# Performance work log

Measured on AMD Instinct MI355X. Metric: run time of the kernel, lower is better.

The kernel has to match this reference:

```python
import jax, jax.numpy as jnp
import numpy as np
import math

N = 100000      # num_of_nodes
E = 1600000     # edges (~avg degree 16)
F = 128         # node_feature
D = 128         # node_hidden (also topK pool size)
NR = 90000      # remaining nodes
L = 2           # num_conv_layer
LAMDA = 0.5
ALPHA = 0.1


def setup_inputs() -> dict:
    key = jax.random.key(0)
    ks = jax.random.split(key, 12)
    g = lambda k, s: jax.random.normal(k, s, jnp.float32) * 0.05
    perm = np.random.RandomState(0).permutation(N)  # disjoint remain/added split
    return {
        "x": jax.random.normal(ks[0], (N, F), jnp.float32),
        "node_scores": jax.random.normal(ks[1], (N,), jnp.float32),
        "W_hid": g(ks[2], (F, D)), "b_hid": jnp.zeros((D,), jnp.float32),
        "Wl": g(ks[3], (D, D)), "bl": jnp.zeros((D,), jnp.float32),
        "Wr": g(ks[4], (D, D)), "br": jnp.zeros((D,), jnp.float32),
        "a": g(ks[5], (1, D)),
        "h0_w": g(ks[6], (D, D)),              # initial_weight (GRU hidden init / GCN weight)
        "W_ih": g(ks[7], (3 * D, D)), "W_hh": g(ks[8], (3 * D, D)),
        "b_ih": jnp.zeros((3 * D,), jnp.float32), "b_hh": jnp.zeros((3 * D,), jnp.float32),
        "edge_index": jax.random.randint(ks[9], (2, E), 0, N),
        "remain_nodes_index": jnp.asarray(perm[:NR], jnp.int32),
        "added_nodes_index": jnp.asarray(perm[NR:], jnp.int32),
        "node_id": jnp.arange(N, dtype=jnp.int32),
    }


def _gru_step(x_in, h, W_ih, W_hh, b_ih, b_hh):
    # torch nn.GRU single step, gate order (r, z, n)
    gx = x_in @ W_ih.T + b_ih
    gh = h @ W_hh.T + b_hh
    xr, xz, xn = jnp.split(gx, 3, axis=-1)
    hr, hz, hn = jnp.split(gh, 3, axis=-1)
    r = jax.nn.sigmoid(xr + hr)
    z = jax.nn.sigmoid(xz + hz)
    n = jnp.tanh(xn + r * hn)
    return (1.0 - z) * n + z * h


def _edge_softmax_weights(edge_index, a, h_l, h_r):
    # _dynamic_self_attention_v2: per-edge scores normalized over src rows
    src, dst = edge_index[0], edge_index[1]
    al = (jax.nn.leaky_relu(h_l, 0.2) * a).sum(-1)   # [N]
    ar = (jax.nn.leaky_relu(h_r, 0.2) * a).sum(-1)   # [N]
    e = al[src] + ar[dst]                            # [E]
    e = jnp.exp(e - e.max())
    rowsum = jax.ops.segment_sum(e, src, num_segments=h_l.shape[0])
    return e / (rowsum[src] + 1e-16)


def _spmm_adj_t(edge_index, w, feats):
    # (A_trans @ feats)[i] = sum over edges with dst==i of w_e * feats[src]
    src, dst = edge_index[0], edge_index[1]
    return jax.ops.segment_sum(w[:, None] * feats[src], dst, num_segments=feats.shape[0])


def reference(x, node_scores, W_hid, b_hid, Wl, bl, Wr, br, a, h0_w, W_ih, W_hh, b_ih, b_hh, edge_index, remain_nodes_index, added_nodes_index, node_id):
    h = jax.nn.relu(x @ W_hid + b_hid)                 # [N, D]
    remain_nodes = node_id[remain_nodes_index]
    remain_x = h[remain_nodes_index]
    added_nodes = node_id[added_nodes_index]
    added_x = h[added_nodes_index]
    scores = node_scores[remain_nodes_index]
    X_res = jnp.zeros((N, D), h.dtype)
    X_res = X_res.at[remain_nodes].set(remain_x).at[added_nodes].set(added_x)
    # topK pooling branch (N > D and NR > D statically)
    _, topk = jax.lax.top_k(scores, D)
    X_pool = remain_x[topk]                            # [D, D]: GRU batch=D, feat=D
    pooling_node = remain_nodes[topk]
    h_new = _gru_step(X_pool, h0_w, W_ih, W_hh, b_ih, b_hh)  # [D, D]
    # torch: X_GCN = X_residual (alias) then in-place scatter -> both updated
    X_res = X_res.at[pooling_node].set(h_new)
    X_gcn = X_res
    Wl_X = jax.nn.relu(X_gcn @ Wl + bl)
    Wr_X = jax.nn.relu(X_gcn @ Wr + br)
    w_edge = _edge_softmax_weights(edge_index, a, Wl_X, Wr_X)
    out = X_gcn
    for l in range(1, L + 1):
        theta = math.log(LAMDA / l + 1.0)
        hi = _spmm_adj_t(edge_index, w_edge, out)
        support = (1.0 - ALPHA) * hi + ALPHA * X_res
        out = jax.nn.relu(theta * (support @ h_new) + (1.0 - theta) * support)
    return out
```

## Files before the change

kernel.cpp:

```cpp
#include <hip/hip_runtime.h>

typedef unsigned int u32;
typedef unsigned short u16;
typedef unsigned long long u64;

#define DD 128
#define ELLW 64
#define NB 196
#define BSH 9
#define BCAP 12288

typedef __attribute__((ext_vector_type(8))) short short8;
typedef __attribute__((ext_vector_type(4))) float f32x4;
union fragu { uint4 q; short8 s; };

__device__ __forceinline__ u32 mono32(float f) {
    u32 u = __float_as_uint(f);
    return (u & 0x80000000u) ? ~u : (u | 0x80000000u);
}
__device__ __forceinline__ u16 f2bf(float f) {
    u32 u = __float_as_uint(f);
    u32 r = (u + 0x7FFFu + ((u >> 16) & 1u)) >> 16;
    return (u16)r;
}
__device__ __forceinline__ float bflo(u32 p) { return __uint_as_float(p << 16); }
__device__ __forceinline__ float bfhi(u32 p) { return __uint_as_float(p & 0xFFFF0000u); }
__device__ __forceinline__ u32 packbf(float a, float b) {
    return (u32)f2bf(a) | ((u32)f2bf(b) << 16);
}

__device__ u32 block_incl_scan(u32 v, u32* wsum ) {
    int t = threadIdx.x, lane = t & 63, wid = t >> 6;
    u32 sc = v;
#pragma unroll
    for (int off = 1; off < 64; off <<= 1) {
        u32 n1 = __shfl_up(sc, off);
        if (lane >= off) sc += n1;
    }
    if (lane == 63) wsum[wid] = sc;
    __syncthreads();
    if (t < 16) {
        u32 wv = wsum[t];
#pragma unroll
        for (int off = 1; off < 16; off <<= 1) {
            u32 n1 = __shfl_up(wv, off, 16);
            if ((t & 15) >= off) wv += n1;
        }
        wsum[t] = wv;
    }
    __syncthreads();
    u32 r = sc + (wid ? wsum[wid - 1] : 0u);
    __syncthreads();
    return r;
}

template <int MODE, int ABF, int EAR>
__global__ __launch_bounds__(256) void k_mfma(
    const void* __restrict__ Ain, const u32* __restrict__ resid,
    const float* __restrict__ B, const float* __restrict__ bias,
    const float* __restrict__ av, const float* __restrict__ scaleS,
    u16* __restrict__ outBF, float* __restrict__ outF, float* __restrict__ outS,
    float theta, int N) {
    __shared__ alignas(16) unsigned char As[64 * 256];
    __shared__ float spart[64];
    int t = threadIdx.x, lane = t & 63, wave = t >> 6;
    int R0 = blockIdx.x * 64;
    int brow = (lane >> 4) * 8;
    int bcol0 = wave * 32 + (lane & 15);
    fragu bfr[2][4];
#pragma unroll
    for (int ntl = 0; ntl < 2; ++ntl)
#pragma unroll
        for (int ks = 0; ks < 4; ++ks) {
            u16 h[8];
#pragma unroll
            for (int i = 0; i < 8; ++i)
                h[i] = f2bf(B[(size_t)(ks * 32 + brow + i) * 128 + bcol0 + ntl * 16]);
            bfr[ntl][ks].q = make_uint4((u32)h[0] | ((u32)h[1] << 16), (u32)h[2] | ((u32)h[3] << 16),
                                        (u32)h[4] | ((u32)h[5] << 16), (u32)h[6] | ((u32)h[7] << 16));
        }
    float bc[2] = {0.f, 0.f}, ac[2] = {0.f, 0.f};
    if (MODE == 0) {
#pragma unroll
        for (int ntl = 0; ntl < 2; ++ntl) {
            bc[ntl] = bias[bcol0 + ntl * 16];
            if (EAR) ac[ntl] = av[bcol0 + ntl * 16];
        }
    }
    if (EAR && t < 64) spart[t] = 0.f;
#pragma unroll
    for (int q2 = 0; q2 < 4; ++q2) {
        int c = t + q2 * 256;
        int row = c >> 4, c16 = c & 15;
        uint4 v = make_uint4(0u, 0u, 0u, 0u);
        if (R0 + row < N) {
            if (ABF == 1) {
                v = ((const uint4*)Ain)[(size_t)(R0 + row) * 16 + c16];
            } else if (ABF == 2) {
                uint4 pv = ((const uint4*)Ain)[(size_t)(R0 + row) * 16 + c16];
                uint4 xv = ((const uint4*)resid)[(size_t)(R0 + row) * 16 + c16];
                v.x = packbf(bflo(pv.x) + 0.1f * bflo(xv.x), bfhi(pv.x) + 0.1f * bfhi(xv.x));
                v.y = packbf(bflo(pv.y) + 0.1f * bflo(xv.y), bfhi(pv.y) + 0.1f * bfhi(xv.y));
                v.z = packbf(bflo(pv.z) + 0.1f * bflo(xv.z), bfhi(pv.z) + 0.1f * bfhi(xv.z));
                v.w = packbf(bflo(pv.w) + 0.1f * bflo(xv.w), bfhi(pv.w) + 0.1f * bfhi(xv.w));
            } else {
                float4 f0 = ((const float4*)Ain)[(size_t)(R0 + row) * 32 + c16 * 2];
                float4 f1 = ((const float4*)Ain)[(size_t)(R0 + row) * 32 + c16 * 2 + 1];
                v.x = packbf(f0.x, f0.y);
                v.y = packbf(f0.z, f0.w);
                v.z = packbf(f1.x, f1.y);
                v.w = packbf(f1.z, f1.w);
            }
        }
        *(uint4*)(As + row * 256 + ((c16 * 16) ^ ((row & 7) << 4))) = v;
    }
    __syncthreads();
    int arow = lane & 15, agrp = lane >> 4;
    float om = 1.f - theta;
#pragma unroll
    for (int rs = 0; rs < 4; ++rs) {
        int rl = rs * 16 + arow;
        fragu afr[4];
#pragma unroll
        for (int ks = 0; ks < 4; ++ks)
            afr[ks].q = *(const uint4*)(As + rl * 256 + ((ks * 64 + agrp * 16) ^ ((rl & 7) << 4)));
        float part[4] = {0.f, 0.f, 0.f, 0.f};
#pragma unroll
        for (int ntl = 0; ntl < 2; ++ntl) {
            f32x4 acc = {0.f, 0.f, 0.f, 0.f};
#pragma unroll
            for (int ks = 0; ks < 4; ++ks)
                acc = __builtin_amdgcn_mfma_f32_16x16x32_bf16(afr[ks].s, bfr[ntl][ks].s, acc, 0, 0, 0);
            int colg = wave * 32 + ntl * 16 + (lane & 15);
#pragma unroll
            for (int r = 0; r < 4; ++r) {
                int rowg = R0 + rs * 16 + agrp * 4 + r;
                if (MODE == 0) {
                    float v = fmaxf(acc[r] + bc[ntl], 0.f);
                    if (rowg < N) outBF[(size_t)rowg * 128 + colg] = f2bf(v);
                    if (EAR) part[r] += v * ac[ntl];
                } else {
                    int rl2 = rs * 16 + agrp * 4 + r;
                    u16 rh = *(const u16*)(As + rl2 * 256 + ((colg * 2) ^ ((rl2 & 7) << 4)));
                    float resv = __uint_as_float((u32)rh << 16);
                    float v = fmaxf(theta * acc[r] + om * resv, 0.f);
                    if (rowg < N) {
                        if (MODE == 2) {
                            float rsc = 1.f / (scaleS[rowg] + 1e-30f);
                            outBF[(size_t)rowg * 128 + colg] = f2bf(v * rsc);
                        } else {
                            outF[(size_t)rowg * 128 + colg] = v;
                        }
                    }
                }
            }
        }
        if (EAR) {
#pragma unroll
            for (int r = 0; r < 4; ++r) {
                float s = part[r];
                s += __shfl_xor(s, 1); s += __shfl_xor(s, 2);
                s += __shfl_xor(s, 4); s += __shfl_xor(s, 8);
                if ((lane & 15) == 0) atomicAdd(&spart[rs * 16 + agrp * 4 + r], s);
            }
        }
    }
    if (EAR) {
        __syncthreads();
        if (t < 64 && R0 + t < N) outS[R0 + t] = expf(spart[t]);
    }
}

__global__ __launch_bounds__(256) void k_spmm(
    const u32* __restrict__ feat, const float* __restrict__ ear,
    const u32* __restrict__ cnt, const int* __restrict__ ell,
    u32* __restrict__ P, int N) {
    int w = (int)((blockIdx.x * (u32)blockDim.x + threadIdx.x) >> 6);
    int lane = threadIdx.x & 63;
    if (w >= N) return;
    int m = (int)min(cnt[w], (u32)ELLW);
    int sv = (lane < m) ? ell[((size_t)w << 6) + lane] : 0;
    float a0 = 0.f, a1 = 0.f;
    int j = 0;
    for (; j + 16 <= m; j += 16) {
        u32 pv[16];
#pragma unroll
        for (int q = 0; q < 16; ++q) {
            int s = __shfl(sv, j + q);
            pv[q] = feat[(size_t)s * 64 + lane];
        }
#pragma unroll
        for (int q = 0; q < 16; ++q) { a0 += bflo(pv[q]); a1 += bfhi(pv[q]); }
    }
    for (; j + 8 <= m; j += 8) {
        u32 pv[8];
#pragma unroll
        for (int q = 0; q < 8; ++q) {
            int s = __shfl(sv, j + q);
            pv[q] = feat[(size_t)s * 64 + lane];
        }
#pragma unroll
        for (int q = 0; q < 8; ++q) { a0 += bflo(pv[q]); a1 += bfhi(pv[q]); }
    }
    for (; j + 2 <= m; j += 2) {
        int s0 = __shfl(sv, j + 0), s1 = __shfl(sv, j + 1);
        u32 p0 = feat[(size_t)s0 * 64 + lane];
        u32 p1 = feat[(size_t)s1 * 64 + lane];
        a0 += bflo(p0) + bflo(p1);
        a1 += bfhi(p0) + bfhi(p1);
    }
    if (j < m) {
        int s0 = __shfl(sv, j);
        u32 p0 = feat[(size_t)s0 * 64 + lane];
        a0 += bflo(p0);
        a1 += bfhi(p0);
    }
    float sc = 0.9f * ear[w];
    P[(size_t)w * 64 + lane] = packbf(sc * a0, sc * a1);
}

__global__ __launch_bounds__(256) void k_bucket(
    const int* __restrict__ ei, u32* __restrict__ bD, u32* __restrict__ bS,
    u32* __restrict__ curD, u32* __restrict__ curS, int E, int nblocks) {
    __shared__ u32 cnt0[NB], cnt1[NB], pos0[NB], pos1[NB], base0[NB], base1[NB];
    int t = threadIdx.x;
    int chunk = (E + nblocks - 1) / nblocks;
    int e0 = blockIdx.x * chunk, e1 = min(E, e0 + chunk);
    for (int i = t; i < NB; i += 256) { cnt0[i] = 0; cnt1[i] = 0; pos0[i] = 0; pos1[i] = 0; }
    __syncthreads();
    for (int e = e0 + t; e < e1; e += 256) {
        int s = ei[e], d = ei[E + e];
        atomicAdd(&cnt0[d >> BSH], 1u);
        atomicAdd(&cnt1[s >> BSH], 1u);
    }
    __syncthreads();
    for (int i = t; i < NB; i += 256) {
        base0[i] = atomicAdd(&curD[i], cnt0[i]);
        base1[i] = atomicAdd(&curS[i], cnt1[i]);
    }
    __syncthreads();
    for (int e = e0 + t; e < e1; e += 256) {
        int s = ei[e], d = ei[E + e];
        int bd = d >> BSH, bs = s >> BSH;
        u32 pD = base0[bd] + atomicAdd(&pos0[bd], 1u);
        u32 pS = base1[bs] + atomicAdd(&pos1[bs], 1u);
        if (pD < (u32)BCAP) bD[(size_t)bd * BCAP + pD] = ((u32)(d & 511) << 17) | (u32)s;
        if (pS < (u32)BCAP) bS[(size_t)bs * BCAP + pS] = ((u32)(s & 511) << 17) | (u32)d;
    }
}

__global__ __launch_bounds__(256) void k_ellSsc(
    const u32* __restrict__ bD, const u32* __restrict__ bS,
    const u32* __restrict__ curD, const u32* __restrict__ curS,
    const float* __restrict__ ear, const u32* __restrict__ Xrbf,
    int* __restrict__ ell, u32* __restrict__ cnt,
    float* __restrict__ S, u32* __restrict__ Xsc, int N) {
    __shared__ u32 lcnt[512];
    __shared__ float ls[512];
    int t = threadIdx.x;
    if (blockIdx.x < NB) {
        int b = blockIdx.x;
        for (int i = t; i < 512; i += 256) lcnt[i] = 0;
        __syncthreads();
        u32 beg = (u32)b * BCAP, end = beg + min(curD[b], (u32)BCAP);
        for (u32 e = beg + t; e < end; e += 256) {
            u32 p = bD[e];
            int dloc = (int)(p >> 17), s = (int)(p & 0x1FFFFu);
            u32 q = atomicAdd(&lcnt[dloc], 1u);
            if (q < (u32)ELLW) ell[(((size_t)(b << BSH) + dloc) << 6) + q] = s;
        }
        __syncthreads();
        int r0 = b << BSH;
        for (int i = t; i < 512; i += 256) {
            int row = r0 + i;
            if (row < N) cnt[row] = min(lcnt[i], (u32)ELLW);
        }
    } else {
        int b = blockIdx.x - NB;
        for (int i = t; i < 512; i += 256) ls[i] = 0.f;
        __syncthreads();
        u32 beg = (u32)b * BCAP, end = beg + min(curS[b], (u32)BCAP);
        for (u32 e = beg + t; e < end; e += 256) {
            u32 p = bS[e];
            int sloc = (int)(p >> 17), d = (int)(p & 0x1FFFFu);
            atomicAdd(&ls[sloc], ear[d]);
        }
        __syncthreads();
        int r0 = b << BSH;
        for (int i = t; i < 512; i += 256) {
            int row = r0 + i;
            if (row < N) S[row] = ls[i];
        }
        int rows = min(512, N - r0);
        if (rows <= 0) return;
        for (int idx = t; idx < rows * 64; idx += 256) {
            int rl = idx >> 6, c = idx & 63;
            int row = r0 + rl;
            float rs = 1.f / (ls[rl] + 1e-30f);
            u32 p = Xrbf[(size_t)row * 64 + c];
            Xsc[(size_t)row * 64 + c] = packbf(bflo(p) * rs, bfhi(p) * rs);
        }
    }
}

__global__ void k_hist(const float* __restrict__ scores, const int* __restrict__ remain,
                       u32* __restrict__ hist, int NR) {
    int i = blockIdx.x * blockDim.x + threadIdx.x;
    if (i < NR) atomicAdd(&hist[mono32(scores[remain[i]]) >> 16], 1u);
}

__global__ void k_cutoff(const u32* __restrict__ hist, u32* __restrict__ misc, int K) {
    __shared__ u32 wsum[16];
    __shared__ u32 carry_s, found_s;
    int t = threadIdx.x;
    if (t == 0) { carry_s = 0; found_s = 0; }
    __syncthreads();
    for (int c = 0; c < 64; ++c) {
        int key = 65535 - ((c << 10) + t);
        u32 v = hist[key];
        u32 carry = carry_s;
        __syncthreads();
        u32 incl = block_incl_scan(v, wsum);
        u32 mycum = carry + incl;
        u32 myprev = mycum - v;
        if (mycum >= (u32)K && myprev < (u32)K) {
            misc[2] = (u32)key;
            misc[3] = myprev;
            found_s = 1;
        }
        if (t == 1023) carry_s = mycum;
        __syncthreads();
        if (found_s) return;
    }
}

__global__ void k_collect(const float* __restrict__ scores, const int* __restrict__ remain,
                          const u32* __restrict__ misc, int* __restrict__ cand,
                          u32* __restrict__ cand_cnt, int NR, int CMAX) {
    u32 B = misc[2];
    int i = blockIdx.x * blockDim.x + threadIdx.x;
    if (i < NR) {
        u32 b = mono32(scores[remain[i]]) >> 16;
        if (b >= B) {
            u32 p = atomicAdd(cand_cnt, 1u);
            if (p < (u32)CMAX) cand[p] = i;
        }
    }
}

__global__ void k_select(const float* __restrict__ scores, const int* __restrict__ remain,
                         const u32* __restrict__ misc, const int* __restrict__ cand,
                         int* __restrict__ pooling, int K, int CMAX) {
    __shared__ u64 keys[4096];
    int n = (int)min(misc[0], (u32)CMAX);
    int t = threadIdx.x;
    for (int c = t; c < n; c += 1024) {
        int i = cand[c];
        u32 m = mono32(scores[remain[i]]);
        keys[c] = ((u64)m << 32) | (u64)(0xFFFFFFFFu - (u32)i);
    }
    __syncthreads();
    for (int c = t; c < n; c += 1024) {
        u64 myk = keys[c];
        int rank = 0;
        for (int j = 0; j < n; ++j) rank += (keys[j] > myk) ? 1 : 0;
        if (rank < K) pooling[rank] = remain[cand[c]];
    }
}

__global__ void k_gru(u32* __restrict__ Xr_bf, const int* __restrict__ pooling,
                      const float* __restrict__ h0w, const float* __restrict__ Wih,
                      const float* __restrict__ Whh, const float* __restrict__ bih,
                      const float* __restrict__ bhh, const float* __restrict__ Wr,
                      const float* __restrict__ br, const float* __restrict__ av,
                      float* __restrict__ hnew, float* __restrict__ ear) {
    __shared__ float xrow[DD], hrow[DD], hn[DD];
    __shared__ float red[2];
    int j = blockIdx.x, t = threadIdx.x;
    int node = pooling[j];
    xrow[t] = __uint_as_float((u32)((const u16*)Xr_bf)[(size_t)node * DD + t] << 16);
    hrow[t] = h0w[j * DD + t];
    __syncthreads();
    float gx[3], gh[3];
#pragma unroll
    for (int g = 0; g < 3; ++g) {
        const float* wi = Wih + (g * DD + t) * DD;
        const float* wh = Whh + (g * DD + t) * DD;
        float ax = bih[g * DD + t];
        float ah = bhh[g * DD + t];
        for (int d = 0; d < DD; ++d) {
            ax += xrow[d] * wi[d];
            ah += hrow[d] * wh[d];
        }
        gx[g] = ax; gh[g] = ah;
    }
    float r = 1.f / (1.f + expf(-(gx[0] + gh[0])));
    float z = 1.f / (1.f + expf(-(gx[1] + gh[1])));
    float nn = tanhf(gx[2] + r * gh[2]);
    float hv = (1.f - z) * nn + z * hrow[t];
    hnew[j * DD + t] = hv;
    hn[t] = hv;
    __syncthreads();
    if (t < 64) Xr_bf[(size_t)node * 64 + t] = packbf(hn[2 * t], hn[2 * t + 1]);
    float acc = br[t];
    for (int k = 0; k < DD; ++k) acc += hn[k] * Wr[k * DD + t];
    float val = fmaxf(acc, 0.f) * av[t];
#pragma unroll
    for (int off = 32; off > 0; off >>= 1) val += __shfl_xor(val, off);
    if ((t & 63) == 0) red[t >> 6] = val;
    __syncthreads();
    if (t == 0) ear[node] = expf(red[0] + red[1]);
}

extern "C" void kernel_launch(void* const* d_in, const int* in_sizes, int n_in,
                              void* d_out, int out_size, void* d_ws, size_t ws_size,
                              hipStream_t stream) {
    const float* x    = (const float*)d_in[0];
    const float* nsc  = (const float*)d_in[1];
    const float* Wh   = (const float*)d_in[2];
    const float* bh   = (const float*)d_in[3];
    const float* Wr   = (const float*)d_in[6];
    const float* br   = (const float*)d_in[7];
    const float* av   = (const float*)d_in[8];
    const float* h0w  = (const float*)d_in[9];
    const float* Wih  = (const float*)d_in[10];
    const float* Whh  = (const float*)d_in[11];
    const float* bih  = (const float*)d_in[12];
    const float* bhh  = (const float*)d_in[13];
    const int* ei     = (const int*)d_in[14];
    const int* remain = (const int*)d_in[15];

    int N = in_sizes[1];
    int E = in_sizes[14] / 2;
    int NR = in_sizes[15];
    const int K = DD;
    const int CMAX = 4096;
    int mblocks = (N + 63) / 64;
    const int NBLK = 512;

    char* ws = (char*)d_ws;
    size_t off = 0;
    auto alloc = [&](size_t bytes) -> size_t {
        off = (off + 255) & ~(size_t)255;
        size_t o = off;
        off += bytes;
        return o;
    };
    size_t bucket_bytes = (size_t)2 * NB * BCAP * 4;
    size_t sup_bytes = (size_t)N * 64 * 4;
    size_t o_Xrbf = alloc((size_t)N * 64 * 4);
    size_t o_Xsc  = alloc((size_t)N * 64 * 4);
    size_t o_Abf  = alloc((size_t)N * 64 * 4);
    size_t o_sup  = alloc(bucket_bytes > sup_bytes ? bucket_bytes : sup_bytes);
    size_t o_ear  = alloc((size_t)N * 4);
    size_t o_ell  = alloc((size_t)N * ELLW * 4);
    size_t o_cand = alloc((size_t)CMAX * 4);
    size_t o_pool = alloc((size_t)K * 4);
    size_t o_hnew = alloc((size_t)DD * DD * 4);
    size_t o_S    = alloc((size_t)N * 4);
    size_t o_cnt  = alloc((size_t)N * 4);
    size_t o_cur  = alloc((size_t)2 * 256 * 4);
    size_t o_hist = alloc((size_t)65536 * 4);
    size_t o_misc = alloc((size_t)64 * 4);
    size_t zero_len = (o_misc + 64 * 4) - o_cur;
    (void)ws_size; (void)n_in; (void)out_size;

    u32*   Xrbf = (u32*)(ws + o_Xrbf);
    u32*   Xsc  = (u32*)(ws + o_Xsc);
    u32*   Abf  = (u32*)(ws + o_Abf);
    u32*   P    = (u32*)(ws + o_sup);
    u32*   bD   = (u32*)(ws + o_sup);
    u32*   bS   = (u32*)(ws + o_sup + (size_t)NB * BCAP * 4);
    float* ear  = (float*)(ws + o_ear);
    int*   ell  = (int*)(ws + o_ell);
    int*   cand = (int*)(ws + o_cand);
    int*   pool = (int*)(ws + o_pool);
    float* hnew = (float*)(ws + o_hnew);
    float* S    = (float*)(ws + o_S);
    u32*   cnt  = (u32*)(ws + o_cnt);
    u32*   curD = (u32*)(ws + o_cur);
    u32*   curS = (u32*)(ws + o_cur + 256 * 4);
    u32*   hist = (u32*)(ws + o_hist);
    u32*   misc = (u32*)(ws + o_misc);

    const float theta1 = 0.40546510810816438f;
    const float theta2 = 0.22314355131420976f;

    hipMemsetAsync(ws + o_cur, 0, zero_len, stream);

    k_mfma<0, 0, 1><<<mblocks, 256, 0, stream>>>(x, nullptr, Wh, bh, av, nullptr,
                                                 (u16*)Xrbf, nullptr, ear, 0.f, N);
    k_hist<<<(NR + 255) / 256, 256, 0, stream>>>(nsc, remain, hist, NR);
    k_cutoff<<<1, 1024, 0, stream>>>(hist, misc, K);
    k_collect<<<(NR + 255) / 256, 256, 0, stream>>>(nsc, remain, misc, cand, misc, NR, CMAX);
    k_select<<<1, 1024, 0, stream>>>(nsc, remain, misc, cand, pool, K, CMAX);
    k_mfma<0, 1, 1><<<mblocks, 256, 0, stream>>>(Xrbf, nullptr, Wr, br, av, nullptr,
                                                 (u16*)Xsc ,
                                                 nullptr, ear, 0.f, N);
    k_gru<<<K, DD, 0, stream>>>(Xrbf, pool, h0w, Wih, Whh, bih, bhh, Wr, br, av, hnew, ear);
    k_bucket<<<NBLK, 256, 0, stream>>>(ei, bD, bS, curD, curS, E, NBLK);
    k_ellSsc<<<2 * NB, 256, 0, stream>>>(bD, bS, curD, curS, ear, Xrbf, ell, cnt, S, Xsc, N);
    k_spmm<<<(N + 3) / 4, 256, 0, stream>>>(Xsc, ear, cnt, ell, P, N);
    k_mfma<2, 2, 0><<<mblocks, 256, 0, stream>>>(P, Xrbf, hnew, nullptr, nullptr, S,
                                                 (u16*)Abf, nullptr, nullptr, theta1, N);
    k_spmm<<<(N + 3) / 4, 256, 0, stream>>>(Abf, ear, cnt, ell, P, N);
    k_mfma<3, 2, 0><<<mblocks, 256, 0, stream>>>(P, Xrbf, hnew, nullptr, nullptr, nullptr,
                                                 nullptr, (float*)d_out, nullptr, theta2, N);
}
```

Before: 384.2 us.

## Fuse hidden and Wr projections; apply inverse row-sum inside SpMM gather

Merges the hidden-layer GEMM and the Wr attention-score GEMM into one kernel that keeps the bf16 hidden tile in shared memory, so the second pass no longer re-reads Xrbf or writes an unused Xsc output. The per-source 1/rowsum scaling is no longer applied by pre-scaling feature copies (the Xsc pass in k_ellSsc and the rescale in the MODE 2 epilogue). Instead each SpMM lane loads invS for its neighbour and the gather uses FMA with a shuffled weight. The 16-wide unrolled gather loop is dropped. This cuts a kernel launch and a full N×128 read/write pass, at the cost of extra invS gathers, shuffles, and some loss of memory-level parallelism in the SpMM.

Measured after the change: 328.4 us (median of 2 runs). 14.5% less time.

```diff
diff --git a/kernel.cpp b/kernel.cpp
--- a/kernel.cpp
+++ b/kernel.cpp
@@ -54,19 +54,18 @@
     return r;
 }
 
-template <int MODE, int ABF, int EAR>
-__global__ __launch_bounds__(256) void k_mfma(
-    const void* __restrict__ Ain, const u32* __restrict__ resid,
-    const float* __restrict__ B, const float* __restrict__ bias,
-    const float* __restrict__ av, const float* __restrict__ scaleS,
-    u16* __restrict__ outBF, float* __restrict__ outF, float* __restrict__ outS,
-    float theta, int N) {
+__global__ __launch_bounds__(256) void k_hid(
+    const float* __restrict__ x, const float* __restrict__ Wh, const float* __restrict__ bh,
+    const float* __restrict__ Wr, const float* __restrict__ br, const float* __restrict__ av,
+    u16* __restrict__ outBF, float* __restrict__ ear, int N) {
     __shared__ alignas(16) unsigned char As[64 * 256];
+    __shared__ alignas(16) unsigned char Xs[64 * 256];
     __shared__ float spart[64];
     int t = threadIdx.x, lane = t & 63, wave = t >> 6;
     int R0 = blockIdx.x * 64;
     int brow = (lane >> 4) * 8;
     int bcol0 = wave * 32 + (lane & 15);
+    if (t < 64) spart[t] = 0.f;
     fragu bfr[2][4];
 #pragma unroll
     for (int ntl = 0; ntl < 2; ++ntl)
@@ -75,48 +74,34 @@
             u16 h[8];
 #pragma unroll
             for (int i = 0; i < 8; ++i)
-                h[i] = f2bf(B[(size_t)(ks * 32 + brow + i) * 128 + bcol0 + ntl * 16]);
+                h[i] = f2bf(Wh[(size_t)(ks * 32 + brow + i) * 128 + bcol0 + ntl * 16]);
             bfr[ntl][ks].q = make_uint4((u32)h[0] | ((u32)h[1] << 16), (u32)h[2] | ((u32)h[3] << 16),
                                         (u32)h[4] | ((u32)h[5] << 16), (u32)h[6] | ((u32)h[7] << 16));
         }
-    float bc[2] = {0.f, 0.f}, ac[2] = {0.f, 0.f};
-    if (MODE == 0) {
-#pragma unroll
-        for (int ntl = 0; ntl < 2; ++ntl) {
-            bc[ntl] = bias[bcol0 + ntl * 16];
-            if (EAR) ac[ntl] = av[bcol0 + ntl * 16];
-        }
-    }
-    if (EAR && t < 64) spart[t] = 0.f;
+    float bc[2], brc[2], avc[2];
+#pragma unroll
+    for (int ntl = 0; ntl < 2; ++ntl) {
+        bc[ntl] = bh[bcol0 + ntl * 16];
+        brc[ntl] = br[bcol0 + ntl * 16];
+        avc[ntl] = av[bcol0 + ntl * 16];
+    }
 #pragma unroll
     for (int q2 = 0; q2 < 4; ++q2) {
         int c = t + q2 * 256;
         int row = c >> 4, c16 = c & 15;
         uint4 v = make_uint4(0u, 0u, 0u, 0u);
         if (R0 + row < N) {
-            if (ABF == 1) {
-                v = ((const uint4*)Ain)[(size_t)(R0 + row) * 16 + c16];
-            } else if (ABF == 2) {
-                uint4 pv = ((const uint4*)Ain)[(size_t)(R0 + row) * 16 + c16];
-                uint4 xv = ((const uint4*)resid)[(size_t)(R0 + row) * 16 + c16];
-                v.x = packbf(bflo(pv.x) + 0.1f * bflo(xv.x), bfhi(pv.x) + 0.1f * bfhi(xv.x));
-                v.y = packbf(bflo(pv.y) + 0.1f * bflo(xv.y), bfhi(pv.y) + 0.1f * bfhi(xv.y));
-                v.z = packbf(bflo(pv.z) + 0.1f * bflo(xv.z), bfhi(pv.z) + 0.1f * bfhi(xv.z));
-                v.w = packbf(bflo(pv.w) + 0.1f * bflo(xv.w), bfhi(pv.w) + 0.1f * bfhi(xv.w));
-            } else {
-                float4 f0 = ((const float4*)Ain)[(size_t)(R0 + row) * 32 + c16 * 2];
-                float4 f1 = ((const float4*)Ain)[(size_t)(R0 + row) * 32 + c16 * 2 + 1];
-                v.x = packbf(f0.x, f0.y);
-                v.y = packbf(f0.z, f0.w);
-                v.z = packbf(f1.x, f1.y);
-                v.w = packbf(f1.z, f1.w);
-            }
+            float4 f0 = ((const float4*)x)[(size_t)(R0 + row) * 32 + c16 * 2];
+            float4 f1 = ((const float4*)x)[(size_t)(R0 + row) * 32 + c16 * 2 + 1];
+            v.x = packbf(f0.x, f0.y);
+            v.y = packbf(f0.z, f0.w);
+            v.z = packbf(f1.x, f1.y);
+            v.w = packbf(f1.z, f1.w);
         }
         *(uint4*)(As + row * 256 + ((c16 * 16) ^ ((row & 7) << 4))) = v;
     }
     __syncthreads();
     int arow = lane & 15, agrp = lane >> 4;
-    float om = 1.f - theta;
 #pragma unroll
     for (int rs = 0; rs < 4; ++rs) {
         int rl = rs * 16 + arow;
@@ -124,7 +109,6 @@
 #pragma unroll
         for (int ks = 0; ks < 4; ++ks)
             afr[ks].q = *(const uint4*)(As + rl * 256 + ((ks * 64 + agrp * 16) ^ ((rl & 7) << 4)));
-        float part[4] = {0.f, 0.f, 0.f, 0.f};
 #pragma unroll
         for (int ntl = 0; ntl < 2; ++ntl) {
             f32x4 acc = {0.f, 0.f, 0.f, 0.f};
@@ -134,86 +118,167 @@
             int colg = wave * 32 + ntl * 16 + (lane & 15);
 #pragma unroll
             for (int r = 0; r < 4; ++r) {
+                int rl2 = rs * 16 + agrp * 4 + r;
+                int rowg = R0 + rl2;
+                float v = fmaxf(acc[r] + bc[ntl], 0.f);
+                u16 hb = f2bf(v);
+                if (rowg < N) outBF[(size_t)rowg * 128 + colg] = hb;
+                *(u16*)(Xs + rl2 * 256 + ((colg * 2) ^ ((rl2 & 7) << 4))) = hb;
+            }
+        }
+    }
+    fragu wfr[2][4];
+#pragma unroll
+    for (int ntl = 0; ntl < 2; ++ntl)
+#pragma unroll
+        for (int ks = 0; ks < 4; ++ks) {
+            u16 h[8];
+#pragma unroll
+            for (int i = 0; i < 8; ++i)
+                h[i] = f2bf(Wr[(size_t)(ks * 32 + brow + i) * 128 + bcol0 + ntl * 16]);
+            wfr[ntl][ks].q = make_uint4((u32)h[0] | ((u32)h[1] << 16), (u32)h[2] | ((u32)h[3] << 16),
+                                        (u32)h[4] | ((u32)h[5] << 16), (u32)h[6] | ((u32)h[7] << 16));
+        }
+    __syncthreads();
+#pragma unroll
+    for (int rs = 0; rs < 4; ++rs) {
+        int rl = rs * 16 + arow;
+        fragu afr[4];
+#pragma unroll
+        for (int ks = 0; ks < 4; ++ks)
+            afr[ks].q = *(const uint4*)(Xs + rl * 256 + ((ks * 64 + agrp * 16) ^ ((rl & 7) << 4)));
+        float part[4] = {0.f, 0.f, 0.f, 0.f};
+#pragma unroll
+        for (int ntl = 0; ntl < 2; ++ntl) {
+            f32x4 acc = {0.f, 0.f, 0.f, 0.f};
+#pragma unroll
+            for (int ks = 0; ks < 4; ++ks)
+                acc = __builtin_amdgcn_mfma_f32_16x16x32_bf16(afr[ks].s, wfr[ntl][ks].s, acc, 0, 0, 0);
+#pragma unroll
+            for (int r = 0; r < 4; ++r)
+                part[r] += fmaxf(acc[r] + brc[ntl], 0.f) * avc[ntl];
+        }
+#pragma unroll
+        for (int r = 0; r < 4; ++r) {
+            float s = part[r];
+            s += __shfl_xor(s, 1); s += __shfl_xor(s, 2);
+            s += __shfl_xor(s, 4); s += __shfl_xor(s, 8);
+            if ((lane & 15) == 0) atomicAdd(&spart[rs * 16 + agrp * 4 + r], s);
+        }
+    }
+    __syncthreads();
+    if (t < 64 && R0 + t < N) ear[R0 + t] = expf(spart[t]);
+}
+
+template <int MODE>
+__global__ __launch_bounds__(256) void k_mfma(
+    const u32* __restrict__ P, const u32* __restrict__ resid,
+    const float* __restrict__ B, u16* __restrict__ outBF, float* __restrict__ outF,
+    float theta, int N) {
+    __shared__ alignas(16) unsigned char As[64 * 256];
+    int t = threadIdx.x, lane = t & 63, wave = t >> 6;
+    int R0 = blockIdx.x * 64;
+    int brow = (lane >> 4) * 8;
+    int bcol0 = wave * 32 + (lane & 15);
+    fragu bfr[2][4];
+#pragma unroll
+    for (int ntl = 0; ntl < 2; ++ntl)
+#pragma unroll
+        for (int ks = 0; ks < 4; ++ks) {
+            u16 h[8];
+#pragma unroll
+            for (int i = 0; i < 8; ++i)
+                h[i] = f2bf(B[(size_t)(ks * 32 + brow + i) * 128 + bcol0 + ntl * 16]);
+            bfr[ntl][ks].q = make_uint4((u32)h[0] | ((u32)h[1] << 16), (u32)h[2] | ((u32)h[3] << 16),
+                                        (u32)h[4] | ((u32)h[5] << 16), (u32)h[6] | ((u32)h[7] << 16));
+        }
+#pragma unroll
+    for (int q2 = 0; q2 < 4; ++q2) {
+        int c = t + q2 * 256;
+        int row = c >> 4, c16 = c & 15;
+        uint4 v = make_uint4(0u, 0u, 0u, 0u);
+        if (R0 + row < N) {
+            uint4 pv = ((const uint4*)P)[(size_t)(R0 + row) * 16 + c16];
+            uint4 xv = ((const uint4*)resid)[(size_t)(R0 + row) * 16 + c16];
+            v.x = packbf(bflo(pv.x) + 0.1f * bflo(xv.x), bfhi(pv.x) + 0.1f * bfhi(xv.x));
+            v.y = packbf(bflo(pv.y) + 0.1f * bflo(xv.y), bfhi(pv.y) + 0.1f * bfhi(xv.y));
+            v.z = packbf(bflo(pv.z) + 0.1f * bflo(xv.z), bfhi(pv.z) + 0.1f * bfhi(xv.z));
+            v.w = packbf(bflo(pv.w) + 0.1f * bflo(xv.w), bfhi(pv.w) + 0.1f * bfhi(xv.w));
+        }
+        *(uint4*)(As + row * 256 + ((c16 * 16) ^ ((row & 7) << 4))) = v;
+    }
+    __syncthreads();
+    int arow = lane & 15, agrp = lane >> 4;
+    float om = 1.f - theta;
+#pragma unroll
+    for (int rs = 0; rs < 4; ++rs) {
+        int rl = rs * 16 + arow;
+        fragu afr[4];
+#pragma unroll
+        for (int ks = 0; ks < 4; ++ks)
+            afr[ks].q = *(const uint4*)(As + rl * 256 + ((ks * 64 + agrp * 16) ^ ((rl & 7) << 4)));
+#pragma unroll
+        for (int ntl = 0; ntl < 2; ++ntl) {
+            f32x4 acc = {0.f, 0.f, 0.f, 0.f};
+#pragma unroll
+            for (int ks = 0; ks < 4; ++ks)
+                acc = __builtin_amdgcn_mfma_f32_16x16x32_bf16(afr[ks].s, bfr[ntl][ks].s, acc, 0, 0, 0);
+            int colg = wave * 32 + ntl * 16 + (lane & 15);
+#pragma unroll
+            for (int r = 0; r < 4; ++r) {
                 int rowg = R0 + rs * 16 + agrp * 4 + r;
-                if (MODE == 0) {
-                    float v = fmaxf(acc[r] + bc[ntl], 0.f);
-                    if (rowg < N) outBF[(size_t)rowg * 128 + colg] = f2bf(v);
-                    if (EAR) part[r] += v * ac[ntl];
-                } else {
-                    int rl2 = rs * 16 + agrp * 4 + r;
-                    u16 rh = *(const u16*)(As + rl2 * 256 + ((colg * 2) ^ ((rl2 & 7) << 4)));
-                    float resv = __uint_as_float((u32)rh << 16);
-                    float v = fmaxf(theta * acc[r] + om * resv, 0.f);
-                    if (rowg < N) {
-                        if (MODE == 2) {
-                            float rsc = 1.f / (scaleS[rowg] + 1e-30f);
-                            outBF[(size_t)rowg * 128 + colg] = f2bf(v * rsc);
-                        } else {
-                            outF[(size_t)rowg * 128 + colg] = v;
-                        }
-                    }
-                }
+                if (rowg >= N) continue;
+                int rl2 = rs * 16 + agrp * 4 + r;
+                u16 rh = *(const u16*)(As + rl2 * 256 + ((colg * 2) ^ ((rl2 & 7) << 4)));
+                float resv = __uint_as_float((u32)rh << 16);
+                float v = fmaxf(theta * acc[r] + om * resv, 0.f);
+                if (MODE == 2) outBF[(size_t)rowg * 128 + colg] = f2bf(v);
+                else outF[(size_t)rowg * 128 + colg] = v;
             }
         }
-        if (EAR) {
-#pragma unroll
-            for (int r = 0; r < 4; ++r) {
-                float s = part[r];
-                s += __shfl_xor(s, 1); s += __shfl_xor(s, 2);
-                s += __shfl_xor(s, 4); s += __shfl_xor(s, 8);
-                if ((lane & 15) == 0) atomicAdd(&spart[rs * 16 + agrp * 4 + r], s);
-            }
-        }
-    }
-    if (EAR) {
-        __syncthreads();
-        if (t < 64 && R0 + t < N) outS[R0 + t] = expf(spart[t]);
     }
 }
 
 __global__ __launch_bounds__(256) void k_spmm(
     const u32* __restrict__ feat, const float* __restrict__ ear,
-    const u32* __restrict__ cnt, const int* __restrict__ ell,
-    u32* __restrict__ P, int N) {
+    const float* __restrict__ invS, const u32* __restrict__ cnt,
+    const int* __restrict__ ell, u32* __restrict__ P, int N) {
     int w = (int)((blockIdx.x * (u32)blockDim.x + threadIdx.x) >> 6);
     int lane = threadIdx.x & 63;
     if (w >= N) return;
     int m = (int)min(cnt[w], (u32)ELLW);
-    int sv = (lane < m) ? ell[((size_t)w << 6) + lane] : 0;
+    int sv = 0; float wv = 0.f;
+    if (lane < m) { sv = ell[((size_t)w << 6) + lane]; wv = invS[sv]; }
     float a0 = 0.f, a1 = 0.f;
     int j = 0;
-    for (; j + 16 <= m; j += 16) {
-        u32 pv[16];
-#pragma unroll
-        for (int q = 0; q < 16; ++q) {
-            int s = __shfl(sv, j + q);
-            pv[q] = feat[(size_t)s * 64 + lane];
-        }
-#pragma unroll
-        for (int q = 0; q < 16; ++q) { a0 += bflo(pv[q]); a1 += bfhi(pv[q]); }
-    }
     for (; j + 8 <= m; j += 8) {
-        u32 pv[8];
+        u32 pv[8]; float wq[8];
 #pragma unroll
         for (int q = 0; q < 8; ++q) {
             int s = __shfl(sv, j + q);
+            wq[q] = __shfl(wv, j + q);
             pv[q] = feat[(size_t)s * 64 + lane];
         }
 #pragma unroll
-        for (int q = 0; q < 8; ++q) { a0 += bflo(pv[q]); a1 += bfhi(pv[q]); }
+        for (int q = 0; q < 8; ++q) {
+            a0 = fmaf(wq[q], bflo(pv[q]), a0);
+            a1 = fmaf(wq[q], bfhi(pv[q]), a1);
+        }
     }
     for (; j + 2 <= m; j += 2) {
         int s0 = __shfl(sv, j + 0), s1 = __shfl(sv, j + 1);
+        float w0 = __shfl(wv, j + 0), w1 = __shfl(wv, j + 1);
         u32 p0 = feat[(size_t)s0 * 64 + lane];
         u32 p1 = feat[(size_t)s1 * 64 + lane];
-        a0 += bflo(p0) + bflo(p1);
-        a1 += bfhi(p0) + bfhi(p1);
+        a0 = fmaf(w0, bflo(p0), fmaf(w1, bflo(p1), a0));
+        a1 = fmaf(w0, bfhi(p0), fmaf(w1, bfhi(p1), a1));
     }
     if (j < m) {
         int s0 = __shfl(sv, j);
+        float w0 = __shfl(wv, j);
         u32 p0 = feat[(size_t)s0 * 64 + lane];
-        a0 += bflo(p0);
-        a1 += bfhi(p0);
+        a0 = fmaf(w0, bflo(p0), a0);
+        a1 = fmaf(w0, bfhi(p0), a1);
     }
     float sc = 0.9f * ear[w];
     P[(size_t)w * 64 + lane] = packbf(sc * a0, sc * a1);
@@ -252,9 +317,8 @@
 __global__ __launch_bounds__(256) void k_ellSsc(
     const u32* __restrict__ bD, const u32* __restrict__ bS,
     const u32* __restrict__ curD, const u32* __restrict__ curS,
-    const float* __restrict__ ear, const u32* __restrict__ Xrbf,
-    int* __restrict__ ell, u32* __restrict__ cnt,
-    float* __restrict__ S, u32* __restrict__ Xsc, int N) {
+    const float* __restrict__ ear,
+    int* __restrict__ ell, u32* __restrict__ cnt, float* __restrict__ invS, int N) {
     __shared__ u32 lcnt[512];
     __shared__ float ls[512];
     int t = threadIdx.x;
@@ -289,16 +353,7 @@
         int r0 = b << BSH;
         for (int i = t; i < 512; i += 256) {
             int row = r0 + i;
-            if (row < N) S[row] = ls[i];
-        }
-        int rows = min(512, N - r0);
-        if (rows <= 0) return;
-        for (int idx = t; idx < rows * 64; idx += 256) {
-            int rl = idx >> 6, c = idx & 63;
-            int row = r0 + rl;
-            float rs = 1.f / (ls[rl] + 1e-30f);
-            u32 p = Xrbf[(size_t)row * 64 + c];
-            Xsc[(size_t)row * 64 + c] = packbf(bflo(p) * rs, bfhi(p) * rs);
+            if (row < N) invS[row] = 1.f / (ls[i] + 1e-30f);
         }
     }
 }
@@ -449,7 +504,6 @@
     size_t bucket_bytes = (size_t)2 * NB * BCAP * 4;
     size_t sup_bytes = (size_t)N * 64 * 4;
     size_t o_Xrbf = alloc((size_t)N * 64 * 4);
-    size_t o_Xsc  = alloc((size_t)N * 64 * 4);
     size_t o_Abf  = alloc((size_t)N * 64 * 4);
     size_t o_sup  = alloc(bucket_bytes > sup_bytes ? bucket_bytes : sup_bytes);
     size_t o_ear  = alloc((size_t)N * 4);
@@ -457,7 +511,7 @@
     size_t o_cand = alloc((size_t)CMAX * 4);
     size_t o_pool = alloc((size_t)K * 4);
     size_t o_hnew = alloc((size_t)DD * DD * 4);
-    size_t o_S    = alloc((size_t)N * 4);
+    size_t o_invS = alloc((size_t)N * 4);
     size_t o_cnt  = alloc((size_t)N * 4);
     size_t o_cur  = alloc((size_t)2 * 256 * 4);
     size_t o_hist = alloc((size_t)65536 * 4);
@@ -466,7 +520,6 @@
     (void)ws_size; (void)n_in; (void)out_size;
 
     u32*   Xrbf = (u32*)(ws + o_Xrbf);
-    u32*   Xsc  = (u32*)(ws + o_Xsc);
     u32*   Abf  = (u32*)(ws + o_Abf);
     u32*   P    = (u32*)(ws + o_sup);
     u32*   bD   = (u32*)(ws + o_sup);
@@ -476,7 +529,7 @@
     int*   cand = (int*)(ws + o_cand);
     int*   pool = (int*)(ws + o_pool);
     float* hnew = (float*)(ws + o_hnew);
-    float* S    = (float*)(ws + o_S);
+    float* invS = (float*)(ws + o_invS);
     u32*   cnt  = (u32*)(ws + o_cnt);
     u32*   curD = (u32*)(ws + o_cur);
     u32*   curS = (u32*)(ws + o_cur + 256 * 4);
@@ -488,22 +541,16 @@
 
     hipMemsetAsync(ws + o_cur, 0, zero_len, stream);
 
-    k_mfma<0, 0, 1><<<mblocks, 256, 0, stream>>>(x, nullptr, Wh, bh, av, nullptr,
-                                                 (u16*)Xrbf, nullptr, ear, 0.f, N);
+    k_hid<<<mblocks, 256, 0, stream>>>(x, Wh, bh, Wr, br, av, (u16*)Xrbf, ear, N);
     k_hist<<<(NR + 255) / 256, 256, 0, stream>>>(nsc, remain, hist, NR);
     k_cutoff<<<1, 1024, 0, stream>>>(hist, misc, K);
     k_collect<<<(NR + 255) / 256, 256, 0, stream>>>(nsc, remain, misc, cand, misc, NR, CMAX);
     k_select<<<1, 1024, 0, stream>>>(nsc, remain, misc, cand, pool, K, CMAX);
-    k_mfma<0, 1, 1><<<mblocks, 256, 0, stream>>>(Xrbf, nullptr, Wr, br, av, nullptr,
-                                                 (u16*)Xsc ,
-                                                 nullptr, ear, 0.f, N);
     k_gru<<<K, DD, 0, stream>>>(Xrbf, pool, h0w, Wih, Whh, bih, bhh, Wr, br, av, hnew, ear);
     k_bucket<<<NBLK, 256, 0, stream>>>(ei, bD, bS, curD, curS, E, NBLK);
-    k_ellSsc<<<2 * NB, 256, 0, stream>>>(bD, bS, curD, curS, ear, Xrbf, ell, cnt, S, Xsc, N);
-    k_spmm<<<(N + 3) / 4, 256, 0, stream>>>(Xsc, ear, cnt, ell, P, N);
-    k_mfma<2, 2, 0><<<mblocks, 256, 0, stream>>>(P, Xrbf, hnew, nullptr, nullptr, S,
-                                                 (u16*)Abf, nullptr, nullptr, theta1, N);
-    k_spmm<<<(N + 3) / 4, 256, 0, stream>>>(Abf, ear, cnt, ell, P, N);
-    k_mfma<3, 2, 0><<<mblocks, 256, 0, stream>>>(P, Xrbf, hnew, nullptr, nullptr, nullptr,
-                                                 nullptr, (float*)d_out, nullptr, theta2, N);
-}
+    k_ellSsc<<<2 * NB, 256, 0, stream>>>(bD, bS, curD, curS, ear, ell, cnt, invS, N);
+    k_spmm<<<(N + 3) / 4, 256, 0, stream>>>(Xrbf, ear, invS, cnt, ell, P, N);
+    k_mfma<2><<<mblocks, 256, 0, stream>>>(P, Xrbf, hnew, (u16*)Abf, nullptr, theta1, N);
+    k_spmm<<<(N + 3) / 4, 256, 0, stream>>>(Abf, ear, invS, cnt, ell, P, N);
+    k_mfma<3><<<mblocks, 256, 0, stream>>>(P, Xrbf, hnew, nullptr, (float*)d_out, theta2, N);
+}
```
